# Kernel tuning notes

Measured on AMD Instinct MI355X. Metric: run time of the kernel, lower is better.

## Reference

```python
import jax, jax.numpy as jnp
import numpy as np

KSIZE = 5
KNUM = 16
STRIDE = 1


def setup_inputs() -> dict:
    key = jax.random.key(0)
    k1, k2 = jax.random.split(key, 2)
    mu_in = jax.random.normal(k1, (16, 28, 28, 1), dtype=jnp.float32)
    # w_mu init: normal(0, 0.05); w_sigma init: constant -2.2 (as in build())
    w_mu = 0.05 * jax.random.normal(k2, (KSIZE, KSIZE, 1, KNUM), dtype=jnp.float32)
    w_sigma = jnp.full((KNUM,), -2.2, dtype=jnp.float32)
    return {"mu_in": mu_in, "w_mu": w_mu, "w_sigma": w_sigma}


def reference(mu_in, w_mu, w_sigma):
    # mu path: standard NHWC conv, VALID padding
    mu_out = jax.lax.conv_general_dilated(
        mu_in, w_mu, window_strides=(STRIDE, STRIDE), padding='VALID',
        dimension_numbers=('NHWC', 'HWIO', 'NHWC'))

    # Sigma path: extract patches -> [B, P, F] matrix (patch ordering is a
    # permutation of TF's, which leaves the Gram matrix X X^T invariant)
    patches = jax.lax.conv_general_dilated_patches(
        mu_in, filter_shape=(KSIZE, KSIZE), window_strides=(STRIDE, STRIDE),
        padding='VALID', dimension_numbers=('NHWC', 'HWIO', 'NHWC'))
    B = mu_in.shape[0]
    X = patches.reshape(B, -1, patches.shape[-1])          # [B, P, F]
    G = jnp.einsum('bpf,bqf->bpq', X, X)                   # [B, P, P]

    # per-output-channel softplus scale, broadcast to [B, P, P, KNUM]
    scale = jnp.log1p(jnp.exp(w_sigma))                    # log(1 + exp(w_sigma))
    Sigma = scale * G[..., None]                           # [B, P, P, KNUM]

    Sigma = jnp.where(jnp.isnan(Sigma), jnp.zeros_like(Sigma), Sigma)
    Sigma = jnp.where(jnp.isinf(Sigma), jnp.zeros_like(Sigma), Sigma)

    # tf.linalg.set_diag acts on the LAST TWO dims -> [P, KNUM] matrices:
    # abs the entries Sigma[:, :, i, i] for i < min(P, KNUM)
    m = min(Sigma.shape[-2], Sigma.shape[-1])
    i = jnp.arange(m)
    Sigma = Sigma.at[..., i, i].set(jnp.abs(Sigma[..., i, i]))
    return (mu_out, Sigma)
```

## Files before the change

kernel.cpp:

```cpp
#include <hip/hip_runtime.h>
#include <math.h>

#define BATCH 16
#define H     28
#define W     28
#define KS    5
#define KN    16
#define OHW   24
#define P     576
#define NTHR  192

#define MU_OUT_ELEMS (BATCH * P * KN)

__global__ __launch_bounds__(NTHR) void vdp_fused_kernel(
    const float* __restrict__ mu_in,
    const float* __restrict__ w_mu,
    const float* __restrict__ w_sigma,
    float* __restrict__ out)
{
    __shared__ float mu_s[H * W];
    __shared__ float sp_s[KN];

    const int bid = blockIdx.x;
    const int b   = bid / P;
    const int p   = bid % P;
    const int tid = threadIdx.x;

    const float* mu_b = mu_in + b * (H * W);
    for (int i = tid; i < H * W; i += NTHR) mu_s[i] = mu_b[i];
    if (tid < KN) sp_s[tid] = log1pf(expf(w_sigma[tid]));
    __syncthreads();

    const int ph = p / OHW;
    const int pw = p % OHW;
    float Xp[KS * KS];
    #pragma unroll
    for (int kh = 0; kh < KS; ++kh)
        #pragma unroll
        for (int kw = 0; kw < KS; ++kw)
            Xp[kh * KS + kw] = mu_s[(ph + kh) * W + (pw + kw)];

    if (tid < KN) {
        float acc = 0.f;
        #pragma unroll
        for (int j = 0; j < KS * KS; ++j)
            acc += Xp[j] * w_mu[j * KN + tid];
        out[(b * P + p) * KN + tid] = acc;
    }

    float* sig = out + MU_OUT_ELEMS;
    const int rowbase = (b * P + p) * P * KN;

    #pragma unroll
    for (int it = 0; it < 3; ++it) {
        const int q  = tid + it * NTHR;
        const int qh = q / OHW;
        const int qw = q % OHW;
        const float* mq = &mu_s[qh * W + qw];

        float g = 0.f;
        #pragma unroll
        for (int kh = 0; kh < KS; ++kh)
            #pragma unroll
            for (int kw = 0; kw < KS; ++kw)
                g += Xp[kh * KS + kw] * mq[kh * W + kw];

        float v[KN];
        #pragma unroll
        for (int k = 0; k < KN; ++k) {
            float val = sp_s[k] * g;
            if (q == k) val = fabsf(val);
            v[k] = val;
        }

        float4* dst = (float4*)(sig + rowbase + q * KN);
        dst[0] = make_float4(v[0],  v[1],  v[2],  v[3]);
        dst[1] = make_float4(v[4],  v[5],  v[6],  v[7]);
        dst[2] = make_float4(v[8],  v[9],  v[10], v[11]);
        dst[3] = make_float4(v[12], v[13], v[14], v[15]);
    }
}

extern "C" void kernel_launch(void* const* d_in, const int* in_sizes, int n_in,
                              void* d_out, int out_size, void* d_ws, size_t ws_size,
                              hipStream_t stream) {
    const float* mu_in   = (const float*)d_in[0];
    const float* w_mu    = (const float*)d_in[1];
    const float* w_sigma = (const float*)d_in[2];
    float* out = (float*)d_out;

    dim3 grid(BATCH * P);
    dim3 block(NTHR);
    vdp_fused_kernel<<<grid, block, 0, stream>>>(mu_in, w_mu, w_sigma, out);
}
```

Measured before the change: 385.8 us.

## Process four rows per block and stage Gram values in shared memory for coalesced stores

Each block now handles four patch rows instead of one, so the shared-memory load of the input image is amortised across rows, and the block size grows to 256 threads. The Gram values for a row are first written to shared memory, then threads emit float4 stores with consecutive threads writing consecutive 16-byte chunks, rather than each thread writing 64 contiguous bytes. The aim is better store coalescing on the large Sigma output, which is bandwidth bound. In exchange it adds two barriers per row and launches a quarter as many blocks.

```diff
diff --git a/kernel.cpp b/kernel.cpp
--- a/kernel.cpp
+++ b/kernel.cpp
@@ -8,8 +8,8 @@
 #define KN    16
 #define OHW   24
 #define P     576
-#define NTHR  192
-
+#define NTHR  256
+#define PPB   4
 #define MU_OUT_ELEMS (BATCH * P * KN)
 
 __global__ __launch_bounds__(NTHR) void vdp_fused_kernel(
@@ -20,64 +20,73 @@
 {
     __shared__ float mu_s[H * W];
     __shared__ float sp_s[KN];
+    __shared__ float g_s[P];
 
-    const int bid = blockIdx.x;
-    const int b   = bid / P;
-    const int p   = bid % P;
-    const int tid = threadIdx.x;
+    const int blocks_per_b = P / PPB;
+    const int b     = blockIdx.x / blocks_per_b;
+    const int pbase = (blockIdx.x % blocks_per_b) * PPB;
+    const int tid   = threadIdx.x;
 
     const float* mu_b = mu_in + b * (H * W);
     for (int i = tid; i < H * W; i += NTHR) mu_s[i] = mu_b[i];
     if (tid < KN) sp_s[tid] = log1pf(expf(w_sigma[tid]));
     __syncthreads();
 
-    const int ph = p / OHW;
-    const int pw = p % OHW;
-    float Xp[KS * KS];
-    #pragma unroll
-    for (int kh = 0; kh < KS; ++kh)
-        #pragma unroll
-        for (int kw = 0; kw < KS; ++kw)
-            Xp[kh * KS + kw] = mu_s[(ph + kh) * W + (pw + kw)];
+    float* sig = out + MU_OUT_ELEMS;
 
-    if (tid < KN) {
-        float acc = 0.f;
-        #pragma unroll
-        for (int j = 0; j < KS * KS; ++j)
-            acc += Xp[j] * w_mu[j * KN + tid];
-        out[(b * P + p) * KN + tid] = acc;
-    }
+    for (int pi = 0; pi < PPB; ++pi) {
+        const int p  = pbase + pi;
+        const int ph = p / OHW;
+        const int pw = p % OHW;
 
-    float* sig = out + MU_OUT_ELEMS;
-    const int rowbase = (b * P + p) * P * KN;
-
-    #pragma unroll
-    for (int it = 0; it < 3; ++it) {
-        const int q  = tid + it * NTHR;
-        const int qh = q / OHW;
-        const int qw = q % OHW;
-        const float* mq = &mu_s[qh * W + qw];
-
-        float g = 0.f;
+        float Xp[KS * KS];
         #pragma unroll
         for (int kh = 0; kh < KS; ++kh)
             #pragma unroll
             for (int kw = 0; kw < KS; ++kw)
-                g += Xp[kh * KS + kw] * mq[kh * W + kw];
+                Xp[kh * KS + kw] = mu_s[(ph + kh) * W + (pw + kw)];
 
-        float v[KN];
-        #pragma unroll
-        for (int k = 0; k < KN; ++k) {
-            float val = sp_s[k] * g;
-            if (q == k) val = fabsf(val);
-            v[k] = val;
+        if (tid < KN) {
+            float acc = 0.f;
+            #pragma unroll
+            for (int j = 0; j < KS * KS; ++j)
+                acc += Xp[j] * w_mu[j * KN + tid];
+            out[(b * P + p) * KN + tid] = acc;
         }
 
-        float4* dst = (float4*)(sig + rowbase + q * KN);
-        dst[0] = make_float4(v[0],  v[1],  v[2],  v[3]);
-        dst[1] = make_float4(v[4],  v[5],  v[6],  v[7]);
-        dst[2] = make_float4(v[8],  v[9],  v[10], v[11]);
-        dst[3] = make_float4(v[12], v[13], v[14], v[15]);
+        for (int q = tid; q < P; q += NTHR) {
+            const int qh = q / OHW;
+            const int qw = q % OHW;
+            const float* mq = &mu_s[qh * W + qw];
+            float g = 0.f;
+            #pragma unroll
+            for (int kh = 0; kh < KS; ++kh)
+                #pragma unroll
+                for (int kw = 0; kw < KS; ++kw)
+                    g += Xp[kh * KS + kw] * mq[kh * W + kw];
+            g_s[q] = g;
+        }
+        __syncthreads();
+
+        float4* rowp = (float4*)(sig + (size_t)(b * P + p) * (P * KN));
+        #pragma unroll
+        for (int j = 0; j < 9; ++j) {
+            const int f = j * NTHR + tid;
+            const int q = f >> 2;
+            const int c = f & 3;
+            const float g = g_s[q];
+            float4 v = make_float4(g * sp_s[4 * c + 0], g * sp_s[4 * c + 1],
+                                   g * sp_s[4 * c + 2], g * sp_s[4 * c + 3]);
+            if (q < KN && (q >> 2) == c) {
+                const int r = q & 3;
+                if (r == 0) v.x = fabsf(v.x);
+                else if (r == 1) v.y = fabsf(v.y);
+                else if (r == 2) v.z = fabsf(v.z);
+                else v.w = fabsf(v.w);
+            }
+            rowp[f] = v;
+        }
+        __syncthreads();
     }
 }
 
@@ -89,7 +98,7 @@
     const float* w_sigma = (const float*)d_in[2];
     float* out = (float*)d_out;
 
-    dim3 grid(BATCH * P);
+    dim3 grid(BATCH * P / PPB);
     dim3 block(NTHR);
     vdp_fused_kernel<<<grid, block, 0, stream>>>(mu_in, w_mu, w_sigma, out);
 }
```

Measured after the change: 351.1 us. 1.1x faster.

## Assign one wave per output row and coalesce Sigma stores via shuffles

Applied to the files above, without the earlier changes.

Each 256-thread block now handles four output rows p, one per 64-lane wave, instead of one row per 192-thread block. Each lane computes nine Gram values, and the values are redistributed with cross-lane shuffles so every store is a contiguous float4 across the wave. w_mu is staged in shared memory. The aim is fully coalesced writes of the large Sigma output and a quarter as many blocks, each loading the image once for four rows. The cost is extra shuffle instructions and more registers per thread.

```diff
diff --git a/kernel.cpp b/kernel.cpp
--- a/kernel.cpp
+++ b/kernel.cpp
@@ -8,8 +8,7 @@
 #define KN    16
 #define OHW   24
 #define P     576
-#define NTHR  192
-
+#define NTHR  256
 #define MU_OUT_ELEMS (BATCH * P * KN)
 
 __global__ __launch_bounds__(NTHR) void vdp_fused_kernel(
@@ -19,20 +18,26 @@
     float* __restrict__ out)
 {
     __shared__ float mu_s[H * W];
+    __shared__ float wmu_s[KS * KS * KN];
     __shared__ float sp_s[KN];
 
-    const int bid = blockIdx.x;
-    const int b   = bid / P;
-    const int p   = bid % P;
-    const int tid = threadIdx.x;
+    const int tid  = threadIdx.x;
+    const int wave = tid >> 6;
+    const int lane = tid & 63;
+
+    const int blocks_per_b = P / 4;
+    const int b = blockIdx.x / blocks_per_b;
+    const int p = (blockIdx.x % blocks_per_b) * 4 + wave;
 
     const float* mu_b = mu_in + b * (H * W);
     for (int i = tid; i < H * W; i += NTHR) mu_s[i] = mu_b[i];
+    for (int i = tid; i < KS * KS * KN; i += NTHR) wmu_s[i] = w_mu[i];
     if (tid < KN) sp_s[tid] = log1pf(expf(w_sigma[tid]));
     __syncthreads();
 
     const int ph = p / OHW;
     const int pw = p % OHW;
+
     float Xp[KS * KS];
     #pragma unroll
     for (int kh = 0; kh < KS; ++kh)
@@ -40,45 +45,55 @@
         for (int kw = 0; kw < KS; ++kw)
             Xp[kh * KS + kw] = mu_s[(ph + kh) * W + (pw + kw)];
 
-    if (tid < KN) {
+    if (lane < KN) {
         float acc = 0.f;
         #pragma unroll
         for (int j = 0; j < KS * KS; ++j)
-            acc += Xp[j] * w_mu[j * KN + tid];
-        out[(b * P + p) * KN + tid] = acc;
+            acc += Xp[j] * wmu_s[j * KN + lane];
+        out[(b * P + p) * KN + lane] = acc;
     }
 
-    float* sig = out + MU_OUT_ELEMS;
-    const int rowbase = (b * P + p) * P * KN;
-
+    float g[9];
     #pragma unroll
-    for (int it = 0; it < 3; ++it) {
-        const int q  = tid + it * NTHR;
+    for (int r = 0; r < 9; ++r) {
+        const int q  = r * 64 + lane;
         const int qh = q / OHW;
         const int qw = q % OHW;
         const float* mq = &mu_s[qh * W + qw];
-
-        float g = 0.f;
+        float acc = 0.f;
         #pragma unroll
         for (int kh = 0; kh < KS; ++kh)
             #pragma unroll
             for (int kw = 0; kw < KS; ++kw)
-                g += Xp[kh * KS + kw] * mq[kh * W + kw];
+                acc += Xp[kh * KS + kw] * mq[kh * W + kw];
+        g[r] = acc;
+    }
 
-        float v[KN];
-        #pragma unroll
-        for (int k = 0; k < KN; ++k) {
-            float val = sp_s[k] * g;
-            if (q == k) val = fabsf(val);
-            v[k] = val;
+    const int c = lane & 3;
+    const float sc0 = sp_s[4 * c + 0];
+    const float sc1 = sp_s[4 * c + 1];
+    const float sc2 = sp_s[4 * c + 2];
+    const float sc3 = sp_s[4 * c + 3];
+
+    float4* rowp = (float4*)(out + MU_OUT_ELEMS + (size_t)(b * P + p) * (P * KN));
+    const int src = 16 * 0 + (lane >> 2);
+    #pragma unroll
+    for (int s = 0; s < 36; ++s) {
+        const float gq = __shfl(g[s >> 2], 16 * (s & 3) + (lane >> 2));
+        float4 v = make_float4(gq * sc0, gq * sc1, gq * sc2, gq * sc3);
+        if (s == 0) {
+            const int q = lane >> 2;
+            if ((q >> 2) == c) {
+                const int r2 = q & 3;
+                if (r2 == 0) v.x = fabsf(v.x);
+                else if (r2 == 1) v.y = fabsf(v.y);
+                else if (r2 == 2) v.z = fabsf(v.z);
+                else v.w = fabsf(v.w);
+            }
         }
-
-        float4* dst = (float4*)(sig + rowbase + q * KN);
-        dst[0] = make_float4(v[0],  v[1],  v[2],  v[3]);
-        dst[1] = make_float4(v[4],  v[5],  v[6],  v[7]);
-        dst[2] = make_float4(v[8],  v[9],  v[10], v[11]);
-        dst[3] = make_float4(v[12], v[13], v[14], v[15]);
+        rowp[s * 64 + lane] = v;
     }
+    (void)src;
 }
 
 extern "C" void kernel_launch(void* const* d_in, const int* in_sizes, int n_in,
@@ -89,7 +104,7 @@
     const float* w_sigma = (const float*)d_in[2];
     float* out = (float*)d_out;
 
-    dim3 grid(BATCH * P);
+    dim3 grid(BATCH * P / 4);
     dim3 block(NTHR);
     vdp_fused_kernel<<<grid, block, 0, stream>>>(mu_in, w_mu, w_sigma, out);
 }
```

Result: faster. 344.7 us (-10.6%).
